# Kernel optimization log

Hardware: AMD Instinct MI355X
Metric: run time of the kernel (lower is better)

Reference implementation:

```python
import jax, jax.numpy as jnp
import numpy as np
from jax import lax

B, C_IN, C_OUT, K, STYLE_DIM, H, W = 16, 128, 128, 3, 512, 128, 128
EPS = 1e-8


def setup_inputs() -> dict:
    key = jax.random.key(0)
    k1, k2, k3, k4 = jax.random.split(key, 4)
    x = jax.random.normal(k1, (B, C_IN, H, W), dtype=jnp.float32)
    style_vector = jax.random.normal(k2, (B, STYLE_DIM), dtype=jnp.float32)
    # EqualizedLR(nn.Linear(style_dim, in_channels)): weight ~ N(0,1), bias = 0
    proj_w = jax.random.normal(k3, (C_IN, STYLE_DIM), dtype=jnp.float32)
    proj_b = jnp.zeros((C_IN,), dtype=jnp.float32)
    # base conv weight (1, out, in, k, k) ~ N(0,1)
    weight = jax.random.normal(k4, (1, C_OUT, C_IN, K, K), dtype=jnp.float32)
    return {"x": x, "style_vector": style_vector, "proj_w": proj_w,
            "proj_b": proj_b, "weight": weight}


def reference(x, style_vector, proj_w, proj_b, weight):
    b = x.shape[0]
    # EqualizedLR: scale input by gain / sqrt(fan_in), gain=1, fan_in=style_dim
    scale = 1.0 / jnp.sqrt(jnp.float32(STYLE_DIM))
    style = (style_vector * scale) @ proj_w.T + proj_b          # [b, in]
    # modulate: [1,out,in,k,k] * [b,1,in,1,1] -> [b,out,in,k,k]
    w = weight * style[:, None, :, None, None]
    # demodulate
    demod = lax.rsqrt(jnp.sum(w * w, axis=(2, 3, 4)) + EPS)     # [b, out]
    w = w * demod[:, :, None, None, None]
    # grouped conv with groups=b == per-sample conv; vmap over batch
    pad = K // 2
    def conv_one(xi, wi):
        # xi: [in,H,W], wi: [out,in,k,k]
        return lax.conv_general_dilated(
            xi[None], wi, window_strides=(1, 1),
            padding=[(pad, pad), (pad, pad)],
            dimension_numbers=("NCHW", "OIHW", "NCHW"))[0]
    out = jax.vmap(conv_one)(x, w)                               # [b,out,H,W]
    return out
```

## Files before the change

### kernel.cpp

```cpp
#include <hip/hip_runtime.h>
#include <cstdint>

#define B_   16
#define CIN  128
#define COUT 128
#define SD   512
#define H_   128
#define W_   128

typedef __bf16 bf16x8  __attribute__((ext_vector_type(8)));
typedef float  floatx4 __attribute__((ext_vector_type(4)));
typedef float floatx16 __attribute__((ext_vector_type(16)));

__global__ void style_kernel(const float* __restrict__ sv, const float* __restrict__ pw,
                             const float* __restrict__ pb, float* __restrict__ style) {
    int bid = blockIdx.x;
    int b = bid >> 7, c = bid & 127;
    int lane = threadIdx.x;
    const float* svb = sv + b * SD;
    const float* pwc = pw + (size_t)c * SD;
    float s = 0.f;
#pragma unroll
    for (int i = 0; i < SD; i += 64) s += svb[i + lane] * pwc[i + lane];
#pragma unroll
    for (int off = 32; off > 0; off >>= 1) s += __shfl_down(s, off, 64);
    if (lane == 0) style[b * CIN + c] = s * 0.044194173824159216f + pb[c];
}

__global__ void modw_kernel(const float* __restrict__ weight, const float* __restrict__ style,
                            __bf16* __restrict__ wmod) {
    int bid = blockIdx.x;
    int b = bid >> 7, o = bid & 127;
    int c = threadIdx.x;
    float s = style[b * CIN + c];
    const float* wp = weight + ((size_t)o * CIN + c) * 9;
    float v[9];
    float ss = 0.f;
#pragma unroll
    for (int t = 0; t < 9; ++t) { v[t] = wp[t] * s; ss += v[t] * v[t]; }
#pragma unroll
    for (int off = 32; off > 0; off >>= 1) ss += __shfl_down(ss, off, 64);
    __shared__ float sh[2];
    int wid = c >> 6, lane = c & 63;
    if (lane == 0) sh[wid] = ss;
    __syncthreads();
    float d = rsqrtf(sh[0] + sh[1] + 1e-8f);
    int chunk = c >> 4, ci = c & 15;
#pragma unroll
    for (int t = 0; t < 9; ++t) {
        wmod[(((((size_t)b * 9 + t) * 8 + chunk) * 128 + o) * 16 + ci)] = (__bf16)(v[t] * d);
    }
}

__global__ __launch_bounds__(256)
void xpose_kernel(const float* __restrict__ x, __bf16* __restrict__ xT) {
    __shared__ uint32_t T[4 * 4 * 8 * 32];
    int ch = blockIdx.x;
    int hq = blockIdx.y;
    int b  = blockIdx.z;
    int t  = threadIdx.x;
    int cp = t >> 5;
    int wq = t & 31;
    int c0 = ch * 16 + cp * 2;
    const float* pa = x + (((size_t)b * CIN + c0    ) * H_ + hq * 4) * W_ + wq * 4;
    const float* pc = x + (((size_t)b * CIN + c0 + 1) * H_ + hq * 4) * W_ + wq * 4;
#pragma unroll
    for (int hr = 0; hr < 4; ++hr) {
        floatx4 va = *(const floatx4*)(pa + (size_t)hr * W_);
        floatx4 vb = *(const floatx4*)(pc + (size_t)hr * W_);
#pragma unroll
        for (int j = 0; j < 4; ++j) {
            uint32_t lo = (uint32_t)__builtin_bit_cast(unsigned short, (__bf16)va[j]);
            uint32_t hi = (uint32_t)__builtin_bit_cast(unsigned short, (__bf16)vb[j]);
            int row = (hr * 4 + j) * 8 + cp;
            T[row * 32 + (wq ^ (row & 31))] = lo | (hi << 16);
        }
    }
    __syncthreads();
    uint32_t* dst = (uint32_t*)xT + ((((size_t)b * 8 + ch) * H_ + hq * 4) * W_) * 8;
#pragma unroll
    for (int it = 0; it < 8; ++it) {
        int o0 = it * 512 + t * 2;
        int cpr = o0 & 7;
        int w   = (o0 >> 3) & 127;
        int hr  = o0 >> 10;
        int r0 = (hr * 4 + (w & 3)) * 8 + cpr;
        uint32_t v0 = T[r0 * 32       + ((w >> 2) ^ (r0 & 31))];
        uint32_t v1 = T[(r0 + 1) * 32 + ((w >> 2) ^ ((r0 + 1) & 31))];
        uint2 pk; pk.x = v0; pk.y = v1;
        *(uint2*)(dst + o0) = pk;
    }
}

#define WXT 66
__global__ __launch_bounds__(256, 2)
void conv_kernel(const __bf16* __restrict__ xT, const __bf16* __restrict__ wmod,
                 float* __restrict__ out) {
    __shared__ __align__(16) __bf16 Xs[2][4 * WXT * 16];
    int w0 = blockIdx.x * 64;
    int h0 = blockIdx.y * 2;
    int b  = blockIdx.z;
    int tid = threadIdx.x;
    int wv = tid >> 6, lane = tid & 63;
    int n = lane & 31, hf = lane >> 5;
    int obase = (wv & 1) * 64;
    int r = wv >> 1;

    floatx16 acc[2][2];
#pragma unroll
    for (int i = 0; i < 2; ++i)
#pragma unroll
        for (int j = 0; j < 2; ++j)
#pragma unroll
            for (int k = 0; k < 16; ++k) acc[i][j][k] = 0.f;

    const __bf16* xb = xT + (size_t)b * 8 * H_ * W_ * 16;

    bool sact[3], sval[3];
    const __bf16* sptr[3];
    int soff[3];
#pragma unroll
    for (int s = 0; s < 3; ++s) {
        int idx = tid + s * 256;
        bool act = (s < 2) || (tid < 16);
        int row = idx / 132;
        int rem = idx - row * 132;
        int wp = rem >> 1, g = rem & 1;
        int hh = h0 - 1 + row, ww = w0 - 1 + wp;
        sact[s] = act;
        sval[s] = act && (unsigned)hh < (unsigned)H_ && (unsigned)ww < (unsigned)W_;
        sptr[s] = xb + ((size_t)hh * W_ + ww) * 16 + g * 8;
        soff[s] = idx * 8;
    }

    bf16x8 sv[3];
#pragma unroll
    for (int s = 0; s < 3; ++s) {
#pragma unroll
        for (int k = 0; k < 8; ++k) sv[s][k] = (__bf16)0.f;
        if (sval[s]) sv[s] = *(const bf16x8*)(sptr[s]);
    }

    const __bf16* apb = wmod + ((((size_t)b * 9) * 8) * 128 + obase + n) * 16 + hf * 8;

    for (int ch = 0; ch < 8; ++ch) {
        bf16x8 a[9][2];
#pragma unroll
        for (int tap = 0; tap < 9; ++tap) {
            const __bf16* ap = apb + tap * 16384 + ch * 2048;
            a[tap][0] = *(const bf16x8*)ap;
            a[tap][1] = *(const bf16x8*)(ap + 512);
        }
        __bf16* xbuf = Xs[ch & 1];
#pragma unroll
        for (int s = 0; s < 3; ++s)
            if (sact[s]) *(bf16x8*)(xbuf + soff[s]) = sv[s];
        if (ch < 7) {
#pragma unroll
            for (int s = 0; s < 3; ++s) {
#pragma unroll
                for (int k = 0; k < 8; ++k) sv[s][k] = (__bf16)0.f;
                if (sval[s]) sv[s] = *(const bf16x8*)(sptr[s] + (size_t)(ch + 1) * (H_ * W_ * 16));
            }
        }
        asm volatile("s_waitcnt lgkmcnt(0)" ::: "memory");
        __builtin_amdgcn_s_barrier();
        asm volatile("" ::: "memory");
#pragma unroll
        for (int tap = 0; tap < 9; ++tap) {
            int kh = tap / 3, kw = tap % 3;
            int row = r + kh;
#pragma unroll
            for (int wt = 0; wt < 2; ++wt) {
                int wp = wt * 32 + n + kw;
                bf16x8 bfrag = *(const bf16x8*)(xbuf + (row * WXT + wp) * 16 + hf * 8);
                acc[0][wt] = __builtin_amdgcn_mfma_f32_32x32x16_bf16(a[tap][0], bfrag, acc[0][wt], 0, 0, 0);
                acc[1][wt] = __builtin_amdgcn_mfma_f32_32x32x16_bf16(a[tap][1], bfrag, acc[1][wt], 0, 0, 0);
            }
        }
    }

    float* ob = out + (((size_t)b * COUT) * H_ + (h0 + r)) * W_ + w0;
#pragma unroll
    for (int i = 0; i < 2; ++i) {
#pragma unroll
        for (int reg = 0; reg < 16; ++reg) {
            int o = obase + i * 32 + (reg & 3) + 8 * (reg >> 2) + 4 * hf;
#pragma unroll
            for (int wt = 0; wt < 2; ++wt)
                __builtin_nontemporal_store(acc[i][wt][reg],
                    &ob[(size_t)o * (H_ * W_) + wt * 32 + n]);
        }
    }
}

extern "C" void kernel_launch(void* const* d_in, const int* in_sizes, int n_in,
                              void* d_out, int out_size, void* d_ws, size_t ws_size,
                              hipStream_t stream) {
    const float* x      = (const float*)d_in[0];
    const float* sv     = (const float*)d_in[1];
    const float* pw     = (const float*)d_in[2];
    const float* pb     = (const float*)d_in[3];
    const float* weight = (const float*)d_in[4];
    float* out = (float*)d_out;

    float*  style = (float*)d_ws;
    __bf16* wmod  = (__bf16*)((char*)d_ws + 8192);
    __bf16* xT    = (__bf16*)((char*)d_ws + 8192 + 4718592);

    style_kernel<<<B_ * CIN, 64, 0, stream>>>(sv, pw, pb, style);
    modw_kernel<<<B_ * COUT, 128, 0, stream>>>(weight, style, wmod);
    xpose_kernel<<<dim3(8, 32, B_), 256, 0, stream>>>(x, xT);
    conv_kernel<<<dim3(2, 64, B_), 256, 0, stream>>>(xT, wmod, out);
}
```

Before: 304.7 us.

## Fuse input transpose and bf16 cast into conv kernel, enlarge row tile

Removes the separate transpose kernel. The conv kernel now reads fp32 NCHW input directly, converts it to bf16 and packs it into shared memory for each channel chunk. Blocks grow to 512 threads covering 4 output rows, which reuses the halo rows across more outputs and halves the block count. The cost is scalar, strided global loads: eight channel-plane loads per thread with no vector width, which may coalesce less well than the old vector loads of the pre-transposed data. Register pressure also rises under launch_bounds(512,4).

```diff
diff --git a/kernel.cpp b/kernel.cpp
--- a/kernel.cpp
+++ b/kernel.cpp
@@ -52,53 +52,13 @@
     }
 }
 
-__global__ __launch_bounds__(256)
-void xpose_kernel(const float* __restrict__ x, __bf16* __restrict__ xT) {
-    __shared__ uint32_t T[4 * 4 * 8 * 32];
-    int ch = blockIdx.x;
-    int hq = blockIdx.y;
-    int b  = blockIdx.z;
-    int t  = threadIdx.x;
-    int cp = t >> 5;
-    int wq = t & 31;
-    int c0 = ch * 16 + cp * 2;
-    const float* pa = x + (((size_t)b * CIN + c0    ) * H_ + hq * 4) * W_ + wq * 4;
-    const float* pc = x + (((size_t)b * CIN + c0 + 1) * H_ + hq * 4) * W_ + wq * 4;
-#pragma unroll
-    for (int hr = 0; hr < 4; ++hr) {
-        floatx4 va = *(const floatx4*)(pa + (size_t)hr * W_);
-        floatx4 vb = *(const floatx4*)(pc + (size_t)hr * W_);
-#pragma unroll
-        for (int j = 0; j < 4; ++j) {
-            uint32_t lo = (uint32_t)__builtin_bit_cast(unsigned short, (__bf16)va[j]);
-            uint32_t hi = (uint32_t)__builtin_bit_cast(unsigned short, (__bf16)vb[j]);
-            int row = (hr * 4 + j) * 8 + cp;
-            T[row * 32 + (wq ^ (row & 31))] = lo | (hi << 16);
-        }
-    }
-    __syncthreads();
-    uint32_t* dst = (uint32_t*)xT + ((((size_t)b * 8 + ch) * H_ + hq * 4) * W_) * 8;
-#pragma unroll
-    for (int it = 0; it < 8; ++it) {
-        int o0 = it * 512 + t * 2;
-        int cpr = o0 & 7;
-        int w   = (o0 >> 3) & 127;
-        int hr  = o0 >> 10;
-        int r0 = (hr * 4 + (w & 3)) * 8 + cpr;
-        uint32_t v0 = T[r0 * 32       + ((w >> 2) ^ (r0 & 31))];
-        uint32_t v1 = T[(r0 + 1) * 32 + ((w >> 2) ^ ((r0 + 1) & 31))];
-        uint2 pk; pk.x = v0; pk.y = v1;
-        *(uint2*)(dst + o0) = pk;
-    }
-}
-
 #define WXT 66
-__global__ __launch_bounds__(256, 2)
-void conv_kernel(const __bf16* __restrict__ xT, const __bf16* __restrict__ wmod,
+__global__ __launch_bounds__(512, 4)
+void conv_kernel(const float* __restrict__ x, const __bf16* __restrict__ wmod,
                  float* __restrict__ out) {
-    __shared__ __align__(16) __bf16 Xs[2][4 * WXT * 16];
+    __shared__ __align__(16) __bf16 Xs[2][6 * WXT * 16];
     int w0 = blockIdx.x * 64;
-    int h0 = blockIdx.y * 2;
+    int h0 = blockIdx.y * 4;
     int b  = blockIdx.z;
     int tid = threadIdx.x;
     int wv = tid >> 6, lane = tid & 63;
@@ -114,34 +74,32 @@
 #pragma unroll
             for (int k = 0; k < 16; ++k) acc[i][j][k] = 0.f;
 
-    const __bf16* xb = xT + (size_t)b * 8 * H_ * W_ * 16;
-
-    bool sact[3], sval[3];
-    const __bf16* sptr[3];
-    int soff[3];
+    bool sact[2], sval[2];
+    const float* sp[2];
+    int soff[2];
 #pragma unroll
-    for (int s = 0; s < 3; ++s) {
-        int idx = tid + s * 256;
-        bool act = (s < 2) || (tid < 16);
-        int row = idx / 132;
-        int rem = idx - row * 132;
-        int wp = rem >> 1, g = rem & 1;
-        int hh = h0 - 1 + row, ww = w0 - 1 + wp;
+    for (int s = 0; s < 2; ++s) {
+        int idx = tid + s * 512;
+        bool act = (s == 0) || (tid < 280);
+        int rr = idx / 132;
+        int rem = idx - rr * 132;
+        int wp = rem >> 1, hfs = rem & 1;
+        int hh = h0 - 1 + rr, ww = w0 - 1 + wp;
+        bool ok = act && (unsigned)hh < (unsigned)H_ && (unsigned)ww < (unsigned)W_;
         sact[s] = act;
-        sval[s] = act && (unsigned)hh < (unsigned)H_ && (unsigned)ww < (unsigned)W_;
-        sptr[s] = xb + ((size_t)hh * W_ + ww) * 16 + g * 8;
+        sval[s] = ok;
+        sp[s] = x + (((size_t)b * CIN + hfs * 8) * H_ + (ok ? hh : 0)) * W_ + (ok ? ww : 0);
         soff[s] = idx * 8;
     }
 
-    bf16x8 sv[3];
+    float sv2[2][8];
 #pragma unroll
-    for (int s = 0; s < 3; ++s) {
+    for (int s = 0; s < 2; ++s)
 #pragma unroll
-        for (int k = 0; k < 8; ++k) sv[s][k] = (__bf16)0.f;
-        if (sval[s]) sv[s] = *(const bf16x8*)(sptr[s]);
-    }
+        for (int j = 0; j < 8; ++j)
+            sv2[s][j] = sval[s] ? sp[s][(size_t)j * (H_ * W_)] : 0.f;
 
-    const __bf16* apb = wmod + ((((size_t)b * 9) * 8) * 128 + obase + n) * 16 + hf * 8;
+    const __bf16* apb = wmod + (size_t)b * 147456 + ((size_t)obase + n) * 16 + hf * 8;
 
     for (int ch = 0; ch < 8; ++ch) {
         bf16x8 a[9][2];
@@ -151,17 +109,28 @@
             a[tap][0] = *(const bf16x8*)ap;
             a[tap][1] = *(const bf16x8*)(ap + 512);
         }
-        __bf16* xbuf = Xs[ch & 1];
+        __bf16* xbuf = &Xs[ch & 1][0];
 #pragma unroll
-        for (int s = 0; s < 3; ++s)
-            if (sact[s]) *(bf16x8*)(xbuf + soff[s]) = sv[s];
+        for (int s = 0; s < 2; ++s) {
+            if (sact[s]) {
+                uint4 pk;
+                uint32_t wds[4];
+#pragma unroll
+                for (int p = 0; p < 4; ++p) {
+                    uint32_t lo = (uint32_t)__builtin_bit_cast(unsigned short, (__bf16)sv2[s][2 * p]);
+                    uint32_t hi = (uint32_t)__builtin_bit_cast(unsigned short, (__bf16)sv2[s][2 * p + 1]);
+                    wds[p] = lo | (hi << 16);
+                }
+                pk.x = wds[0]; pk.y = wds[1]; pk.z = wds[2]; pk.w = wds[3];
+                *(uint4*)(xbuf + soff[s]) = pk;
+            }
+        }
         if (ch < 7) {
 #pragma unroll
-            for (int s = 0; s < 3; ++s) {
+            for (int s = 0; s < 2; ++s)
 #pragma unroll
-                for (int k = 0; k < 8; ++k) sv[s][k] = (__bf16)0.f;
-                if (sval[s]) sv[s] = *(const bf16x8*)(sptr[s] + (size_t)(ch + 1) * (H_ * W_ * 16));
-            }
+                for (int j = 0; j < 8; ++j)
+                    sv2[s][j] = sval[s] ? sp[s][((size_t)(ch + 1) * 16 + j) * (H_ * W_)] : 0.f;
         }
         asm volatile("s_waitcnt lgkmcnt(0)" ::: "memory");
         __builtin_amdgcn_s_barrier();
@@ -206,10 +175,8 @@
 
     float*  style = (float*)d_ws;
     __bf16* wmod  = (__bf16*)((char*)d_ws + 8192);
-    __bf16* xT    = (__bf16*)((char*)d_ws + 8192 + 4718592);
 
     style_kernel<<<B_ * CIN, 64, 0, stream>>>(sv, pw, pb, style);
     modw_kernel<<<B_ * COUT, 128, 0, stream>>>(weight, style, wmod);
-    xpose_kernel<<<dim3(8, 32, B_), 256, 0, stream>>>(x, xT);
-    conv_kernel<<<dim3(2, 64, B_), 256, 0, stream>>>(xT, wmod, out);
+    conv_kernel<<<dim3(2, 32, B_), 512, 0, stream>>>(x, wmod, out);
 }
```

Measured after the change: 620.8 us. 104% more time.
